# Kernel optimization log

Measured on AMD Instinct MI355X. Metric: run time of the kernel, lower is better.

Reference implementation:

```python
import jax, jax.numpy as jnp
import numpy as np

B, N, N_FEAT = 16, 1024, 128
N_LAYER, AGG_HIDDEN, FC_HIDDEN, N_CLASS = 3, 64, 128, 10
NEG_INF = -9e15
LEAKY_SLOPE = 0.2


def setup_inputs() -> dict:
    key = jax.random.key(0)
    ks = jax.random.split(key, 8)
    x = jax.random.normal(ks[0], (B, N, N_FEAT), dtype=jnp.float32)
    adj = jax.random.randint(ks[1], (B, N, N), 0, 2).astype(jnp.float32)
    # per-layer GAT params, stacked over layers
    Ws = jax.random.normal(ks[2], (N_LAYER, N_FEAT, AGG_HIDDEN), dtype=jnp.float32) * 0.1
    a1 = jax.random.normal(ks[3], (N_LAYER, AGG_HIDDEN), dtype=jnp.float32) * 0.1
    a2 = jax.random.normal(ks[4], (N_LAYER, AGG_HIDDEN), dtype=jnp.float32) * 0.1
    W1 = jax.random.normal(ks[5], (AGG_HIDDEN * N_LAYER, FC_HIDDEN), dtype=jnp.float32) * 0.05
    b1 = jnp.zeros((FC_HIDDEN,), dtype=jnp.float32)
    W2 = jax.random.normal(ks[6], (FC_HIDDEN, N_CLASS), dtype=jnp.float32) * 0.05
    b2 = jnp.zeros((N_CLASS,), dtype=jnp.float32)
    return {"x": x, "adj": adj, "Ws": Ws, "a1": a1, "a2": a2,
            "W1": W1, "b1": b1, "W2": W2, "b2": b2}


def _gat_layer(x, adj, W, a1, a2):
    # h: [B, N, H]
    h = jnp.einsum('bnf,fh->bnh', x, W)
    # e_ij = LeakyReLU(a1.h_i + a2.h_j)  -- split-a trick, avoids [B,N,N,2H]
    f1 = jnp.einsum('bnh,h->bn', h, a1)
    f2 = jnp.einsum('bnh,h->bn', h, a2)
    e = jax.nn.leaky_relu(f1[:, :, None] + f2[:, None, :], LEAKY_SLOPE)  # [B,N,N]
    att = jax.nn.softmax(jnp.where(adj > 0, e, NEG_INF), axis=-1)
    return jnp.einsum('bnm,bmh->bnh', att, h)


def reference(x, adj, Ws, a1, a2, W1, b1, W2, b2):
    # eval mode: dropout is identity
    outs = [jax.nn.relu(_gat_layer(x, adj, Ws[i], a1[i], a2[i]))
            for i in range(N_LAYER)]
    h = jnp.concatenate(outs, axis=2)          # [B, N, H*L]
    pooled = jnp.mean(h, axis=1)               # 'avg' pool over nodes -> [B, H*L]
    z = jax.nn.relu(pooled @ W1 + b1)
    return jax.nn.softmax(z @ W2 + b2, axis=-1)  # [B, n_class]
```

## Files before the change

### kernel.cpp

```cpp
#include <hip/hip_runtime.h>

#define B 16
#define N 1024
#define NF 128
#define NL 3
#define AH 64
#define HC 192
#define FCH 128
#define NC 10
#define L2E 1.44269504088896f

typedef __attribute__((ext_vector_type(8))) short bf16x8;
typedef __attribute__((ext_vector_type(4))) float f32x4;
typedef __attribute__((ext_vector_type(4))) unsigned int u32x4;

static __device__ __forceinline__ unsigned short f2bf(float f) {
  unsigned int x = __builtin_bit_cast(unsigned int, f);
  return (unsigned short)((x + 0x7fffu + ((x >> 16) & 1u)) >> 16);
}
static __device__ __forceinline__ float bf2f(unsigned short u) {
  unsigned int x = ((unsigned int)u) << 16;
  return __builtin_bit_cast(float, x);
}

__global__ __launch_bounds__(256) void k_mask(
    const float* __restrict__ adj, unsigned short* __restrict__ mskf,
    float* __restrict__ pooled)
{
  __shared__ unsigned short sm[16][66];
  const int t = threadIdx.x;
  const int stripe = blockIdx.x;
  const float* ap = adj + (size_t)stripe * 16 * N;

  if (stripe == 0) {
    #pragma unroll
    for (int i = 0; i < 12; ++i) pooled[i * 256 + t] = 0.f;
  }

  #pragma unroll
  for (int c = 0; c < 4; ++c) {
    const int row = c * 4 + (t >> 6);
    const int j0 = (t & 63) * 16;
    const float* p = ap + (size_t)row * N + j0;
    unsigned int bits = 0;
    #pragma unroll
    for (int q = 0; q < 4; ++q) {
      const uint4 u = *(const uint4*)(p + q * 4);
      bits |= (u.x ? 1u : 0u) << (q * 4 + 0);
      bits |= (u.y ? 1u : 0u) << (q * 4 + 1);
      bits |= (u.z ? 1u : 0u) << (q * 4 + 2);
      bits |= (u.w ? 1u : 0u) << (q * 4 + 3);
    }
    sm[row][t & 63] = (unsigned short)bits;
  }
  __syncthreads();

  #pragma unroll
  for (int cc = 0; cc < 4; ++cc) {
    const int o = cc * 256 + t;
    const int jt = o >> 6, lane_o = o & 63;
    const int lr = lane_o & 15, lg = lane_o >> 4;
    const int sh = (lg & 1) * 8;
    const unsigned int b0 = (sm[lr][jt * 4 + (lg >> 1)] >> sh) & 0xffu;
    const unsigned int b1 = (sm[lr][jt * 4 + 2 + (lg >> 1)] >> sh) & 0xffu;
    mskf[(size_t)stripe * 1024 + o] = (unsigned short)(b0 | (b1 << 8));
  }
}

__global__ __launch_bounds__(256, 2) void k_feat(
    const float* __restrict__ x, const float* __restrict__ Ws,
    const float* __restrict__ a1, const float* __restrict__ a2,
    unsigned short* __restrict__ h_f, float* __restrict__ f1g,
    float* __restrict__ f2g)
{
  __shared__ float xs[64][132];
  __shared__ unsigned short wl[2][64][136];
  unsigned short (*hlds)[72] = (unsigned short(*)[72])&xs[0][0];
  const int t = threadIdx.x;
  const int n0g = blockIdx.x * 64;
  const int gb = n0g >> 10, nl0 = n0g & 1023;
  const int wv = t >> 6, lane = t & 63;
  const int lr = lane & 15, lg = lane >> 4;
  const int lrow = wv * 16 + lr;
  const int wcol = t & 63, woct = t >> 6;

#define LOADW(R, L) {                                                         \
    _Pragma("unroll")                                                         \
    for (int p = 0; p < 4; ++p) {                                             \
      const int oct = p * 4 + woct;                                           \
      _Pragma("unroll")                                                       \
      for (int i = 0; i < 8; ++i)                                             \
        R[p][i] = Ws[((size_t)(L) * NF + oct * 8 + i) * AH + wcol];           \
    } }
#define WRITEW(R) {                                                           \
    _Pragma("unroll")                                                         \
    for (int p = 0; p < 4; ++p) {                                             \
      const int oct = p * 4 + woct;                                           \
      bf16x8 hv, lv;                                                          \
      _Pragma("unroll")                                                       \
      for (int i = 0; i < 8; ++i) {                                           \
        const unsigned short hi = f2bf(R[p][i]);                              \
        hv[i] = (short)hi;                                                    \
        lv[i] = (short)f2bf(R[p][i] - bf2f(hi));                              \
      }                                                                       \
      *(bf16x8*)&wl[0][wcol][oct * 8] = hv;                                   \
      *(bf16x8*)&wl[1][wcol][oct * 8] = lv;                                   \
    } }
#define MFMAL(L) {                                                            \
    _Pragma("unroll")                                                         \
    for (int n2 = 0; n2 < 4; ++n2) {                                          \
      const int n = (L) * 4 + n2;                                             \
      _Pragma("unroll")                                                       \
      for (int kf = 0; kf < 4; ++kf) {                                        \
        const bf16x8 whi = *(const bf16x8*)&wl[0][n2 * 16 + lr][kf * 32 + lg * 8]; \
        const bf16x8 wlo = *(const bf16x8*)&wl[1][n2 * 16 + lr][kf * 32 + lg * 8]; \
        acc[n] = __builtin_amdgcn_mfma_f32_16x16x32_bf16(xhi[kf], whi, acc[n], 0, 0, 0); \
        acc[n] = __builtin_amdgcn_mfma_f32_16x16x32_bf16(xhi[kf], wlo, acc[n], 0, 0, 0); \
        acc[n] = __builtin_amdgcn_mfma_f32_16x16x32_bf16(xlo[kf], whi, acc[n], 0, 0, 0); \
      }                                                                       \
    } }

  float wrA[4][8], wrB[4][8];
  LOADW(wrA, 0);

  #pragma unroll
  for (int p = 0; p < 8; ++p) {
    const int q = p * 256 + t;
    const int row = q >> 5, c4 = (q & 31) * 4;
    *(float4*)&xs[row][c4] = *(const float4*)&x[(size_t)(n0g + row) * NF + c4];
  }
  __syncthreads();

  bf16x8 xhi[4], xlo[4];
  #pragma unroll
  for (int kf = 0; kf < 4; ++kf) {
    const float4 q0 = *(const float4*)&xs[lrow][kf * 32 + lg * 8];
    const float4 q1 = *(const float4*)&xs[lrow][kf * 32 + lg * 8 + 4];
    const float xv[8] = {q0.x, q0.y, q0.z, q0.w, q1.x, q1.y, q1.z, q1.w};
    #pragma unroll
    for (int e = 0; e < 8; ++e) {
      const unsigned short hi = f2bf(xv[e]);
      xhi[kf][e] = (short)hi;
      xlo[kf][e] = (short)f2bf(xv[e] - bf2f(hi));
    }
  }

  f32x4 acc[12];
  #pragma unroll
  for (int n = 0; n < 12; ++n) acc[n] = (f32x4){0.f, 0.f, 0.f, 0.f};

  WRITEW(wrA);
  LOADW(wrB, 1);
  __syncthreads();
  MFMAL(0);
  __syncthreads();
  WRITEW(wrB);
  LOADW(wrA, 2);
  __syncthreads();
  MFMAL(1);
  __syncthreads();
  WRITEW(wrA);
  __syncthreads();
  MFMAL(2);

#undef LOADW
#undef WRITEW
#undef MFMAL

  float s1[3][4], s2[3][4];
  #pragma unroll
  for (int l = 0; l < 3; ++l)
    #pragma unroll
    for (int r = 0; r < 4; ++r) { s1[l][r] = 0.f; s2[l][r] = 0.f; }
  #pragma unroll
  for (int n = 0; n < 12; ++n) {
    const int col = n * 16 + lr;
    const float a1v = a1[col] * L2E, a2v = a2[col] * L2E;
    const int l = n >> 2;
    #pragma unroll
    for (int r = 0; r < 4; ++r) {
      s1[l][r] += acc[n][r] * a1v;
      s2[l][r] += acc[n][r] * a2v;
    }
  }
  #pragma unroll
  for (int off = 1; off < 16; off <<= 1)
    #pragma unroll
    for (int l = 0; l < 3; ++l)
      #pragma unroll
      for (int r = 0; r < 4; ++r) {
        s1[l][r] += __shfl_xor(s1[l][r], off);
        s2[l][r] += __shfl_xor(s2[l][r], off);
      }
  if (lr == 0) {
    #pragma unroll
    for (int l = 0; l < 3; ++l)
      #pragma unroll
      for (int r = 0; r < 4; ++r) {
        const int rw = n0g + wv * 16 + lg * 4 + r;
        f1g[(size_t)l * (B * N) + rw] = s1[l][r];
        f2g[(size_t)l * (B * N) + rw] = s2[l][r];
      }
  }

  __syncthreads();
  #pragma unroll
  for (int n = 0; n < 12; ++n) {
    const int col = n * 16 + lr;
    #pragma unroll
    for (int rp = 0; rp < 2; ++rp) {
      const unsigned int pr = (unsigned int)f2bf(acc[n][rp * 2]) |
                              ((unsigned int)f2bf(acc[n][rp * 2 + 1]) << 16);
      *(unsigned int*)&hlds[col][wv * 16 + lg * 4 + rp * 2] = pr;
    }
  }
  __syncthreads();
  #pragma unroll
  for (int p = 0; p < 6; ++p) {
    const int widx = p * 256 + t;
    const int lane_w = widx & 63;
    const int jb2 = (widx >> 6) & 1;
    const int n_w = (widx >> 7) & 3;
    const int l_w = widx >> 9;
    const int col = l_w * 64 + n_w * 16 + (lane_w & 15);
    const int jloc = jb2 * 32 + (lane_w >> 4) * 8;
    const size_t off =
        ((((size_t)(gb * 3 + l_w) * 4 + n_w) * 32 + (nl0 >> 5) + jb2) * 64 + lane_w) * 8;
    *(uint4*)&h_f[off] = *(const uint4*)&hlds[col][jloc];
  }
}

__global__ __launch_bounds__(192, 3) void k_att(
    const unsigned short* __restrict__ mskf, const unsigned short* __restrict__ h_f,
    const float* __restrict__ f1, const float* __restrict__ f2,
    float* __restrict__ pooled)
{
  const int bid = blockIdx.x;
  const int blk = (bid & 7) * 128 + (bid >> 3);
  const int b = blk >> 6;
  const int i0 = (blk & 63) * 16;
  const int ph = ((bid * 5) & 7) * 128;
  const int t = threadIdx.x;
  const int l = t >> 6, lane = t & 63;
  const int lr = lane & 15, lg = lane >> 4;

  __shared__ float uvt[NL][2][N];

  const float* f2p = f2 + (size_t)l * (B * N) + b * N;
  float mx = -1e30f;
  #pragma unroll
  for (int ch = 0; ch < 4; ++ch) {
    const int jb = ch * 256 + lane * 4;
    const float4 q = *(const float4*)&f2p[jb];
    mx = fmaxf(mx, fmaxf(fmaxf(q.x, q.y), fmaxf(q.z, q.w)));
    *(float4*)&uvt[l][0][jb] =
        (float4){exp2f(q.x), exp2f(q.y), exp2f(q.z), exp2f(q.w)};
    *(float4*)&uvt[l][1][jb] =
        (float4){exp2f(0.2f * q.x), exp2f(0.2f * q.y), exp2f(0.2f * q.z), exp2f(0.2f * q.w)};
  }
  #pragma unroll
  for (int off = 1; off < 64; off <<= 1) mx = fmaxf(mx, __shfl_xor(mx, off));

  const float f1r = f1[(size_t)l * (B * N) + b * N + i0 + lr];
  const float tts = f1r + mx;
  const float sr = fmaxf(tts, 0.f) + 0.2f * fminf(tts, 0.f);
  const float A = exp2f(f1r - sr);
  const float C = exp2f(0.2f * f1r - sr);

  const unsigned short* hfb = h_f + ((size_t)(b * 3 + l)) * 65536;
  const unsigned short* mrow = mskf + ((size_t)(b * 64 + (i0 >> 4))) * 1024;
  const float* ut = &uvt[l][0][0];
  const float* vt = &uvt[l][1][0];
  const bf16x8 ones = {(short)0x3F80, (short)0x3F80, (short)0x3F80, (short)0x3F80,
                       (short)0x3F80, (short)0x3F80, (short)0x3F80, (short)0x3F80};

  f32x4 acc[4];
  #pragma unroll
  for (int n = 0; n < 4; ++n) acc[n] = (f32x4){0.f, 0.f, 0.f, 0.f};
  f32x4 accd = (f32x4){0.f, 0.f, 0.f, 0.f};

#define LOADJ(BUF, MW, J) {                                                   \
    const int jj = (J) & (N - 1);                                             \
    MW = (unsigned int)mrow[(jj >> 6) * 64 + lane];                           \
    _Pragma("unroll")                                                         \
    for (int q = 0; q < 8; ++q) {                                             \
      const int ks = q >> 2, n = q & 3;                                       \
      BUF[q] = *(const bf16x8*)&hfb[(((size_t)n * 32 + (jj >> 5) + ks) * 64 + \
                                     lane) * 8];                              \
    } }

#define COMPJ(BUF, MW, J) {                                                   \
    _Pragma("unroll")                                                         \
    for (int ks = 0; ks < 2; ++ks) {                                          \
      const int kb = ((J) & (N - 1)) + ks * 32 + lg * 8;                      \
      const float4 u0 = *(const float4*)&ut[kb];                              \
      const float4 u1 = *(const float4*)&ut[kb + 4];                          \
      const float4 v0 = *(const float4*)&vt[kb];                              \
      const float4 v1 = *(const float4*)&vt[kb + 4];                          \
      const unsigned int mby = ((MW) >> (ks * 8)) & 0xffu;                    \
      const float uu[8] = {u0.x, u0.y, u0.z, u0.w, u1.x, u1.y, u1.z, u1.w};   \
      const float vv[8] = {v0.x, v0.y, v0.z, v0.w, v1.x, v1.y, v1.z, v1.w};   \
      unsigned int pk[4];                                                     \
      _Pragma("unroll")                                                       \
      for (int ep = 0; ep < 4; ++ep) {                                        \
        unsigned int pr[2];                                                   \
        _Pragma("unroll")                                                     \
        for (int h = 0; h < 2; ++h) {                                         \
          const int e = ep * 2 + h;                                           \
                  \
          const float p = fmaxf(A * uu[e], C * vv[e]);                        \
                  \
          const unsigned int sel =                                            \
              (unsigned int)(((int)(mby << (31 - e))) >> 31);                 \
          pr[h] = (__builtin_bit_cast(unsigned int, p) + 0x8000u) & sel;      \
        }                                                                     \
        pk[ep] = __builtin_amdgcn_perm(pr[1], pr[0], 0x07060302u);            \
      }                                                                       \
      const u32x4 pkv = {pk[0], pk[1], pk[2], pk[3]};                         \
      const bf16x8 av = __builtin_bit_cast(bf16x8, pkv);                      \
      _Pragma("unroll")                                                       \
      for (int n = 0; n < 4; ++n)                                             \
        acc[n] = __builtin_amdgcn_mfma_f32_16x16x32_bf16(av, BUF[ks * 4 + n], \
                                                         acc[n], 0, 0, 0);    \
      accd = __builtin_amdgcn_mfma_f32_16x16x32_bf16(av, ones, accd, 0, 0, 0);\
    } }

#define SBAR __builtin_amdgcn_sched_barrier(0)

  bf16x8 bA[8], bB[8];
  unsigned int mwA, mwB;
  LOADJ(bA, mwA, ph);
  SBAR;
  for (int j0 = 0; j0 < N; j0 += 128) {
    LOADJ(bB, mwB, ph + j0 + 64);
    SBAR;
    COMPJ(bA, mwA, ph + j0);
    SBAR;
    LOADJ(bA, mwA, ph + j0 + 128);
    SBAR;
    COMPJ(bB, mwB, ph + j0 + 64);
    SBAR;
  }
#undef LOADJ
#undef COMPJ
#undef SBAR

  float dn[4];
  #pragma unroll
  for (int r = 0; r < 4; ++r) dn[r] = 1.f / fmaxf(accd[r], 1e-37f);

  #pragma unroll
  for (int n = 0; n < 4; ++n) {
    float csum = 0.f;
    #pragma unroll
    for (int r = 0; r < 4; ++r) csum += fmaxf(acc[n][r] * dn[r], 0.f);
    csum += __shfl_xor(csum, 16);
    csum += __shfl_xor(csum, 32);
    if (lg == 0) atomicAdd(&pooled[b * HC + l * 64 + n * 16 + lr], csum);
  }
}

__global__ __launch_bounds__(192) void k_head(
    const float* __restrict__ pooled_sums, const float* __restrict__ W1,
    const float* __restrict__ b1, const float* __restrict__ W2,
    const float* __restrict__ b2, float* __restrict__ out)
{
  const int b = blockIdx.x, t = threadIdx.x;
  __shared__ float pooled[HC];
  __shared__ float z[FCH];
  __shared__ float logits[NC];

  if (t < HC) pooled[t] = pooled_sums[b * HC + t] * (1.f / (float)N);
  __syncthreads();

  if (t < FCH) {
    float a = b1[t];
    #pragma unroll 4
    for (int f = 0; f < HC; ++f) a += pooled[f] * W1[(size_t)f * FCH + t];
    z[t] = a > 0.f ? a : 0.f;
  }
  __syncthreads();

  if (t < NC) {
    float a = b2[t];
    #pragma unroll 4
    for (int f = 0; f < FCH; ++f) a += z[f] * W2[(size_t)f * NC + t];
    logits[t] = a;
  }
  __syncthreads();

  if (t == 0) {
    float mxl = logits[0];
    for (int c = 1; c < NC; ++c) mxl = fmaxf(mxl, logits[c]);
    float e[NC], sum = 0.f;
    for (int c = 0; c < NC; ++c) { e[c] = __expf(logits[c] - mxl); sum += e[c]; }
    const float inv = 1.f / sum;
    for (int c = 0; c < NC; ++c) out[b * NC + c] = e[c] * inv;
  }
}

extern "C" void kernel_launch(void* const* d_in, const int* in_sizes, int n_in,
                              void* d_out, int out_size, void* d_ws, size_t ws_size,
                              hipStream_t stream)
{
  const float* x   = (const float*)d_in[0];
  const float* adj = (const float*)d_in[1];
  const float* Ws  = (const float*)d_in[2];
  const float* a1  = (const float*)d_in[3];
  const float* a2  = (const float*)d_in[4];
  const float* W1  = (const float*)d_in[5];
  const float* b1  = (const float*)d_in[6];
  const float* W2  = (const float*)d_in[7];
  const float* b2  = (const float*)d_in[8];
  float* out = (float*)d_out;

  unsigned short* h_f   = (unsigned short*)d_ws;
  float*          f1    = (float*)(h_f + (size_t)B * HC * N);
  float*          f2    = f1 + (size_t)NL * B * N;
  float*          pooled= f2 + (size_t)NL * B * N;
  unsigned short* mskf  = (unsigned short*)(pooled + B * HC + 16);

  k_mask<<<B * 64, 256, 0, stream>>>(adj, mskf, pooled);
  k_feat<<<256, 256, 0, stream>>>(x, Ws, a1, a2, h_f, f1, f2);
  k_att <<<1024, 192, 0, stream>>>(mskf, h_f, f1, f2, pooled);
  k_head<<<B, 192, 0, stream>>>(pooled, W1, b1, W2, b2, out);
}
```

Measured before the change: 69.48 us.

## Restructure attention kernel to one wave per layer with 32 rows per block

k_att now launches single-wave blocks, each handling one GAT layer and 32 query rows (two 16-row tiles) instead of three waves covering three layers for 16 rows. Each loaded h/bf16 B-fragment and u/v LDS value is reused for two row tiles, which halves global h traffic per row and amortizes the f2 exp table setup over more rows. In exchange, register pressure rises from doubled accumulators, and blocks are smaller with fewer total waves (1536 waves vs 3072), which may reduce latency hiding.

```diff
diff --git a/kernel.cpp b/kernel.cpp
--- a/kernel.cpp
+++ b/kernel.cpp
@@ -230,21 +230,22 @@
   }
 }
 
-__global__ __launch_bounds__(192, 3) void k_att(
+__global__ __launch_bounds__(64, 3) void k_att(
     const unsigned short* __restrict__ mskf, const unsigned short* __restrict__ h_f,
     const float* __restrict__ f1, const float* __restrict__ f2,
     float* __restrict__ pooled)
 {
   const int bid = blockIdx.x;
-  const int blk = (bid & 7) * 128 + (bid >> 3);
-  const int b = blk >> 6;
-  const int i0 = (blk & 63) * 16;
+  const int blk = (bid & 7) * 192 + (bid >> 3);
+  const int b = blk / 96;
+  const int rem = blk - b * 96;
+  const int l = rem >> 5;
+  const int i0 = (rem & 31) * 32;
   const int ph = ((bid * 5) & 7) * 128;
-  const int t = threadIdx.x;
-  const int l = t >> 6, lane = t & 63;
+  const int lane = threadIdx.x;
   const int lr = lane & 15, lg = lane >> 4;
 
-  __shared__ float uvt[NL][2][N];
+  __shared__ float uvt[2][N];
 
   const float* f2p = f2 + (size_t)l * (B * N) + b * N;
   float mx = -1e30f;
@@ -253,35 +254,42 @@
     const int jb = ch * 256 + lane * 4;
     const float4 q = *(const float4*)&f2p[jb];
     mx = fmaxf(mx, fmaxf(fmaxf(q.x, q.y), fmaxf(q.z, q.w)));
-    *(float4*)&uvt[l][0][jb] =
+    *(float4*)&uvt[0][jb] =
         (float4){exp2f(q.x), exp2f(q.y), exp2f(q.z), exp2f(q.w)};
-    *(float4*)&uvt[l][1][jb] =
+    *(float4*)&uvt[1][jb] =
         (float4){exp2f(0.2f * q.x), exp2f(0.2f * q.y), exp2f(0.2f * q.z), exp2f(0.2f * q.w)};
   }
   #pragma unroll
   for (int off = 1; off < 64; off <<= 1) mx = fmaxf(mx, __shfl_xor(mx, off));
 
-  const float f1r = f1[(size_t)l * (B * N) + b * N + i0 + lr];
-  const float tts = f1r + mx;
-  const float sr = fmaxf(tts, 0.f) + 0.2f * fminf(tts, 0.f);
-  const float A = exp2f(f1r - sr);
-  const float C = exp2f(0.2f * f1r - sr);
+  const float f1r0 = f1[(size_t)l * (B * N) + b * N + i0 + lr];
+  const float f1r1 = f1[(size_t)l * (B * N) + b * N + i0 + 16 + lr];
+  const float tt0 = f1r0 + mx, tt1 = f1r1 + mx;
+  const float sr0 = fmaxf(tt0, 0.f) + 0.2f * fminf(tt0, 0.f);
+  const float sr1 = fmaxf(tt1, 0.f) + 0.2f * fminf(tt1, 0.f);
+  const float A0 = exp2f(f1r0 - sr0), C0 = exp2f(0.2f * f1r0 - sr0);
+  const float A1 = exp2f(f1r1 - sr1), C1 = exp2f(0.2f * f1r1 - sr1);
 
   const unsigned short* hfb = h_f + ((size_t)(b * 3 + l)) * 65536;
   const unsigned short* mrow = mskf + ((size_t)(b * 64 + (i0 >> 4))) * 1024;
-  const float* ut = &uvt[l][0][0];
-  const float* vt = &uvt[l][1][0];
+  const float* ut = &uvt[0][0];
+  const float* vt = &uvt[1][0];
   const bf16x8 ones = {(short)0x3F80, (short)0x3F80, (short)0x3F80, (short)0x3F80,
                        (short)0x3F80, (short)0x3F80, (short)0x3F80, (short)0x3F80};
 
-  f32x4 acc[4];
-  #pragma unroll
-  for (int n = 0; n < 4; ++n) acc[n] = (f32x4){0.f, 0.f, 0.f, 0.f};
-  f32x4 accd = (f32x4){0.f, 0.f, 0.f, 0.f};
-
-#define LOADJ(BUF, MW, J) {                                                   \
+  f32x4 acc0[4], acc1[4];
+  #pragma unroll
+  for (int n = 0; n < 4; ++n) {
+    acc0[n] = (f32x4){0.f, 0.f, 0.f, 0.f};
+    acc1[n] = (f32x4){0.f, 0.f, 0.f, 0.f};
+  }
+  f32x4 accd0 = (f32x4){0.f, 0.f, 0.f, 0.f};
+  f32x4 accd1 = (f32x4){0.f, 0.f, 0.f, 0.f};
+
+#define LOADJ(BUF, MW0, MW1, J) {                                             \
     const int jj = (J) & (N - 1);                                             \
-    MW = (unsigned int)mrow[(jj >> 6) * 64 + lane];                           \
+    MW0 = (unsigned int)mrow[(jj >> 6) * 64 + lane];                          \
+    MW1 = (unsigned int)mrow[1024 + (jj >> 6) * 64 + lane];                   \
     _Pragma("unroll")                                                         \
     for (int q = 0; q < 8; ++q) {                                             \
       const int ks = q >> 2, n = q & 3;                                       \
@@ -289,7 +297,26 @@
                                      lane) * 8];                              \
     } }
 
-#define COMPJ(BUF, MW, J) {                                                   \
+#define PGEN(AV, Aw, Cw, MB) {                                                \
+    unsigned int pk[4];                                                       \
+    _Pragma("unroll")                                                         \
+    for (int ep = 0; ep < 4; ++ep) {                                          \
+      unsigned int pr[2];                                                     \
+      _Pragma("unroll")                                                       \
+      for (int h = 0; h < 2; ++h) {                                           \
+        const int e = ep * 2 + h;                                             \
+        const float p = fmaxf((Aw) * uu[e], (Cw) * vv[e]);                    \
+        const unsigned int sel =                                              \
+            (unsigned int)(((int)((MB) << (31 - e))) >> 31);                  \
+        pr[h] = (__builtin_bit_cast(unsigned int, p) + 0x8000u) & sel;        \
+      }                                                                       \
+      pk[ep] = __builtin_amdgcn_perm(pr[1], pr[0], 0x07060302u);              \
+    }                                                                         \
+    const u32x4 pkv = {pk[0], pk[1], pk[2], pk[3]};                           \
+    AV = __builtin_bit_cast(bf16x8, pkv);                                     \
+  }
+
+#define COMPJ(BUF, MW0, MW1, J) {                                             \
     _Pragma("unroll")                                                         \
     for (int ks = 0; ks < 2; ++ks) {                                          \
       const int kb = ((J) & (N - 1)) + ks * 32 + lg * 8;                      \
@@ -297,63 +324,60 @@
       const float4 u1 = *(const float4*)&ut[kb + 4];                          \
       const float4 v0 = *(const float4*)&vt[kb];                              \
       const float4 v1 = *(const float4*)&vt[kb + 4];                          \
-      const unsigned int mby = ((MW) >> (ks * 8)) & 0xffu;                    \
+      const unsigned int mb0 = ((MW0) >> (ks * 8)) & 0xffu;                   \
+      const unsigned int mb1 = ((MW1) >> (ks * 8)) & 0xffu;                   \
       const float uu[8] = {u0.x, u0.y, u0.z, u0.w, u1.x, u1.y, u1.z, u1.w};   \
       const float vv[8] = {v0.x, v0.y, v0.z, v0.w, v1.x, v1.y, v1.z, v1.w};   \
-      unsigned int pk[4];                                                     \
+      bf16x8 av0, av1;                                                        \
+      PGEN(av0, A0, C0, mb0);                                                 \
+      PGEN(av1, A1, C1, mb1);                                                 \
       _Pragma("unroll")                                                       \
-      for (int ep = 0; ep < 4; ++ep) {                                        \
-        unsigned int pr[2];                                                   \
-        _Pragma("unroll")                                                     \
-        for (int h = 0; h < 2; ++h) {                                         \
-          const int e = ep * 2 + h;                                           \
-                  \
-          const float p = fmaxf(A * uu[e], C * vv[e]);                        \
-                  \
-          const unsigned int sel =                                            \
-              (unsigned int)(((int)(mby << (31 - e))) >> 31);                 \
-          pr[h] = (__builtin_bit_cast(unsigned int, p) + 0x8000u) & sel;      \
-        }                                                                     \
-        pk[ep] = __builtin_amdgcn_perm(pr[1], pr[0], 0x07060302u);            \
+      for (int n = 0; n < 4; ++n) {                                           \
+        acc0[n] = __builtin_amdgcn_mfma_f32_16x16x32_bf16(av0, BUF[ks * 4 + n],\
+                                                          acc0[n], 0, 0, 0);  \
+        acc1[n] = __builtin_amdgcn_mfma_f32_16x16x32_bf16(av1, BUF[ks * 4 + n],\
+                                                          acc1[n], 0, 0, 0);  \
       }                                                                       \
-      const u32x4 pkv = {pk[0], pk[1], pk[2], pk[3]};                         \
-      const bf16x8 av = __builtin_bit_cast(bf16x8, pkv);                      \
-      _Pragma("unroll")                                                       \
-      for (int n = 0; n < 4; ++n)                                             \
-        acc[n] = __builtin_amdgcn_mfma_f32_16x16x32_bf16(av, BUF[ks * 4 + n], \
-                                                         acc[n], 0, 0, 0);    \
-      accd = __builtin_amdgcn_mfma_f32_16x16x32_bf16(av, ones, accd, 0, 0, 0);\
+      accd0 = __builtin_amdgcn_mfma_f32_16x16x32_bf16(av0, ones, accd0, 0, 0, 0);\
+      accd1 = __builtin_amdgcn_mfma_f32_16x16x32_bf16(av1, ones, accd1, 0, 0, 0);\
     } }
 
 #define SBAR __builtin_amdgcn_sched_barrier(0)
 
   bf16x8 bA[8], bB[8];
-  unsigned int mwA, mwB;
-  LOADJ(bA, mwA, ph);
+  unsigned int mwA0, mwA1, mwB0, mwB1;
+  LOADJ(bA, mwA0, mwA1, ph);
   SBAR;
   for (int j0 = 0; j0 < N; j0 += 128) {
-    LOADJ(bB, mwB, ph + j0 + 64);
+    LOADJ(bB, mwB0, mwB1, ph + j0 + 64);
     SBAR;
-    COMPJ(bA, mwA, ph + j0);
+    COMPJ(bA, mwA0, mwA1, ph + j0);
     SBAR;
-    LOADJ(bA, mwA, ph + j0 + 128);
+    LOADJ(bA, mwA0, mwA1, ph + j0 + 128);
     SBAR;
-    COMPJ(bB, mwB, ph + j0 + 64);
+    COMPJ(bB, mwB0, mwB1, ph + j0 + 64);
     SBAR;
   }
 #undef LOADJ
+#undef PGEN
 #undef COMPJ
 #undef SBAR
 
-  float dn[4];
-  #pragma unroll
-  for (int r = 0; r < 4; ++r) dn[r] = 1.f / fmaxf(accd[r], 1e-37f);
+  float dn0[4], dn1[4];
+  #pragma unroll
+  for (int r = 0; r < 4; ++r) {
+    dn0[r] = 1.f / fmaxf(accd0[r], 1e-37f);
+    dn1[r] = 1.f / fmaxf(accd1[r], 1e-37f);
+  }
 
   #pragma unroll
   for (int n = 0; n < 4; ++n) {
     float csum = 0.f;
     #pragma unroll
-    for (int r = 0; r < 4; ++r) csum += fmaxf(acc[n][r] * dn[r], 0.f);
+    for (int r = 0; r < 4; ++r) {
+      csum += fmaxf(acc0[n][r] * dn0[r], 0.f);
+      csum += fmaxf(acc1[n][r] * dn1[r], 0.f);
+    }
     csum += __shfl_xor(csum, 16);
     csum += __shfl_xor(csum, 32);
     if (lg == 0) atomicAdd(&pooled[b * HC + l * 64 + n * 16 + lr], csum);
@@ -422,6 +446,6 @@
 
   k_mask<<<B * 64, 256, 0, stream>>>(adj, mskf, pooled);
   k_feat<<<256, 256, 0, stream>>>(x, Ws, a1, a2, h_f, f1, f2);
-  k_att <<<1024, 192, 0, stream>>>(mskf, h_f, f1, f2, pooled);
+  k_att <<<B * 32 * 3, 64, 0, stream>>>(mskf, h_f, f1, f2, pooled);
   k_head<<<B, 192, 0, stream>>>(pooled, W1, b1, W2, b2, out);
 }
```

Measured after the change: 68.08 us. -2.0%, faster.
